# Kernel tuning notes

Measured on AMD Instinct MI355X. Metric: run time of the kernel, lower is better.

## Reference

```python
import jax, jax.numpy as jnp
import numpy as np

B, N, EDGES = 16, 50000, 1600000
CLAMP_MIN, CLAMP_MAX = -10.0, 10.0
EPS = 1e-6


def setup_inputs() -> dict:
    key = jax.random.key(0)
    ks = jax.random.split(key, 8)
    return {
        "chem_influence": jax.random.normal(ks[0], (B, N), dtype=jnp.float32),
        "E": jax.random.normal(ks[1], (B, N), dtype=jnp.float32),
        "o_pre": jax.random.uniform(ks[2], (B, N), dtype=jnp.float32),
        "w": jax.random.normal(ks[3], (EDGES,), dtype=jnp.float32),
        "threshold": jax.random.uniform(ks[4], (N,), dtype=jnp.float32),
        "decay": jax.random.uniform(ks[5], (N,), dtype=jnp.float32),
        "src": jax.random.randint(ks[6], (EDGES,), 0, N, dtype=jnp.int32),
        "dst": jax.random.randint(ks[7], (EDGES,), 0, N, dtype=jnp.int32),
    }


def reference(chem_influence, E, o_pre, w, threshold, decay, src, dst):
    # Gap-junction currents: gather, sign-compare, weighted scatter-add.
    Oj = o_pre[:, src]                      # (B, EDGES) presynaptic outputs
    En = E[:, dst]                          # (B, EDGES) postsynaptic internal states
    sgn = jnp.where(Oj >= En, 1.0, -1.0)
    contrib = Oj * w * sgn                  # (B, EDGES)
    gj_sum = jnp.zeros_like(chem_influence).at[:, dst].add(contrib)  # (B, N)

    # Neuron dynamics (eqs 10, 11).
    S = jnp.clip(E + chem_influence + gj_sum, CLAMP_MIN, CLAMP_MAX)
    gt = S > threshold                      # broadcast (N,) over (B, N)
    mask = (~gt) & (jnp.abs(S - E) <= EPS)
    new_o = jax.nn.relu(S - threshold)
    new_e = jnp.where(gt, new_o, jnp.where(mask, E - decay, S))
    return (new_o, new_e)
```

## Files before the change

### kernel.cpp

```cpp
#include <hip/hip_runtime.h>

#define BATCH 16
#define NNODES 50000
#define NEDGES 1600000
#define BN (BATCH * NNODES)
#define CLAMP_LO -10.0f
#define CLAMP_HI 10.0f
#define EPS_V 1e-6f

#define BSZ 64
#define NBINS 782
#define CAPE 2816
#define RPT 11
#define NBLK_P 782
#define EPB 2048

__global__ __launch_bounds__(256) void prep_fused(
    const float* __restrict__ o_pre,
    const int* __restrict__ src, const int* __restrict__ dst,
    const float* __restrict__ w,
    float* __restrict__ o_t,
    uint2* __restrict__ binned, int* __restrict__ gcur) {
    __shared__ int lh[NBINS];
    const int tid = threadIdx.x, bid = blockIdx.x;
    for (int i = tid; i < NBINS; i += 256) lh[i] = 0;

    const int4*   dst4 = (const int4*)dst;
    const int4*   src4 = (const int4*)src;
    const float4* w4   = (const float4*)w;
    const int e4base = bid * (EPB / 4);
    int4 d[2], s[2];
    float4 ww[2];
    bool val[2];
#pragma unroll
    for (int j = 0; j < 2; ++j) {
        int i4 = e4base + j * 256 + tid;
        val[j] = (i4 < NEDGES / 4);
        if (val[j]) { d[j] = dst4[i4]; s[j] = src4[i4]; ww[j] = w4[i4]; }
    }

    {
        int t = bid * 64 + (tid >> 2);
        int q = tid & 3;
        if (t < NNODES) {
            float v0 = o_pre[(q * 4 + 0) * NNODES + t];
            float v1 = o_pre[(q * 4 + 1) * NNODES + t];
            float v2 = o_pre[(q * 4 + 2) * NNODES + t];
            float v3 = o_pre[(q * 4 + 3) * NNODES + t];
            *(float4*)(o_t + (size_t)t * BATCH + q * 4) =
                make_float4(v0, v1, v2, v3);
        }
    }
    __syncthreads();

#pragma unroll
    for (int j = 0; j < 2; ++j) {
        if (val[j]) {
            atomicAdd(&lh[d[j].x >> 6], 1);
            atomicAdd(&lh[d[j].y >> 6], 1);
            atomicAdd(&lh[d[j].z >> 6], 1);
            atomicAdd(&lh[d[j].w >> 6], 1);
        }
    }
    __syncthreads();

    for (int i = tid; i < NBINS; i += 256) {
        int c = lh[i];
        int base = c ? atomicAdd(&gcur[i], c) : 0;
        lh[i] = i * CAPE + base;
    }
    __syncthreads();

#pragma unroll
    for (int j = 0; j < 2; ++j) {
        if (val[j]) {
            int   dd[4] = {d[j].x, d[j].y, d[j].z, d[j].w};
            int   ss[4] = {s[j].x, s[j].y, s[j].z, s[j].w};
            float wv[4] = {ww[j].x, ww[j].y, ww[j].z, ww[j].w};
#pragma unroll
            for (int m = 0; m < 4; ++m) {
                int dn  = dd[m];
                int bin = dn >> 6;
                int pos = atomicAdd(&lh[bin], 1);
                if (pos < (bin + 1) * CAPE)
                    binned[pos] = make_uint2(
                        (unsigned)ss[m] | ((unsigned)(dn & 63) << 16),
                        __float_as_uint(wv[m]));
            }
        }
    }
}

__global__ __launch_bounds__(256, 4) void bin_gather7(
    const float* __restrict__ o_t, const float* __restrict__ E,
    const float* __restrict__ chem, const float* __restrict__ threshold,
    const float* __restrict__ decay, const int* __restrict__ gcur,
    const uint2* __restrict__ binned,
    float* __restrict__ out_o, float* __restrict__ out_e) {
    __shared__ int   cnt_l[BSZ];
    __shared__ int   offs[BSZ + 1];
    __shared__ uint2 eb[CAPE];
    const int k = blockIdx.x, tid = threadIdx.x;
    const int node0 = k * BSZ;
    const int nn = (NNODES - node0 < BSZ) ? (NNODES - node0) : BSZ;
    const int s0 = k * CAPE;
    int cnt = gcur[k];
    if (cnt > CAPE) cnt = CAPE;

    uint2 r[RPT];
    if (tid < BSZ) cnt_l[tid] = 0;
    __syncthreads();
#pragma unroll
    for (int j = 0; j < RPT; ++j) {
        int idx = tid + j * 256;
        if (idx < cnt) {
            uint2 p = binned[s0 + idx];
            r[j] = p;
            atomicAdd(&cnt_l[(p.x >> 16) & 63], 1);
        }
    }
    __syncthreads();

    if (tid < BSZ) {
        int c = cnt_l[tid];
        int v = c;
#pragma unroll
        for (int o = 1; o < BSZ; o <<= 1) {
            int u = __shfl_up(v, o);
            if (tid >= o) v += u;
        }
        offs[tid]  = v - c;
        cnt_l[tid] = v - c;
        if (tid == BSZ - 1) offs[BSZ] = cnt;
    }
    __syncthreads();

#pragma unroll
    for (int j = 0; j < RPT; ++j) {
        int idx = tid + j * 256;
        if (idx < cnt) {
            uint2 p = r[j];
            int pos = atomicAdd(&cnt_l[(p.x >> 16) & 63], 1);
            eb[pos] = p;
        }
    }
    __syncthreads();

    if (tid < nn * 4) {
        const int n  = tid >> 2;
        const int q4 = (tid & 3) * 4;
        const int gn = node0 + n;
        const int e0 = offs[n], e1 = offs[n + 1];
        float ev[4];
#pragma unroll
        for (int j = 0; j < 4; ++j) ev[j] = E[(q4 + j) * NNODES + gn];
        const float th = threshold[gn];
        const float dc = decay[gn];
        float ch[4];
#pragma unroll
        for (int j = 0; j < 4; ++j) ch[j] = chem[(q4 + j) * NNODES + gn];

        float4 acc = make_float4(0.f, 0.f, 0.f, 0.f);
#define ACC1(P)                                                                 \
        {                                                                       \
            float4 oj = *(const float4*)(o_t + (size_t)((P).x & 0xFFFFu) * BATCH + q4); \
            float wv = __uint_as_float((P).y), nwv = -wv;                       \
            acc.x = fmaf(oj.x, (oj.x >= ev[0]) ? wv : nwv, acc.x);              \
            acc.y = fmaf(oj.y, (oj.y >= ev[1]) ? wv : nwv, acc.y);              \
            acc.z = fmaf(oj.z, (oj.z >= ev[2]) ? wv : nwv, acc.z);              \
            acc.w = fmaf(oj.w, (oj.w >= ev[3]) ? wv : nwv, acc.w);              \
        }
        int i = e0;
        for (; i + 4 <= e1; i += 4) {
            uint2 p0 = eb[i];
            uint2 p1 = eb[i + 1];
            uint2 p2 = eb[i + 2];
            uint2 p3 = eb[i + 3];
            ACC1(p0); ACC1(p1); ACC1(p2); ACC1(p3);
        }
        for (; i < e1; ++i) {
            uint2 p0 = eb[i];
            ACC1(p0);
        }
#undef ACC1

        float av[4] = {acc.x, acc.y, acc.z, acc.w};
#pragma unroll
        for (int j = 0; j < 4; ++j) {
            float e = ev[j];
            float S = e + ch[j] + av[j];
            S = fminf(fmaxf(S, CLAMP_LO), CLAMP_HI);
            float no = fmaxf(S - th, 0.0f);
            float ne;
            if (S > th) ne = no;
            else if (fabsf(S - e) <= EPS_V) ne = e - dc;
            else ne = S;
            out_o[(q4 + j) * NNODES + gn] = no;
            out_e[(q4 + j) * NNODES + gn] = ne;
        }
    }
}

__global__ void edge_scatter_dev(const float* __restrict__ o_pre, const float* __restrict__ E,
                                 const float* __restrict__ w, const int* __restrict__ src,
                                 const int* __restrict__ dst, float* __restrict__ gj) {
    int e = blockIdx.x * blockDim.x + threadIdx.x;
    if (e >= NEDGES) return;
    int s = src[e];
    int d = dst[e];
    float wv = w[e];
#pragma unroll
    for (int b = 0; b < BATCH; ++b) {
        float oj = o_pre[b * NNODES + s];
        float en = E[b * NNODES + d];
        atomicAdd(&gj[b * NNODES + d], (oj >= en) ? oj * wv : -oj * wv);
    }
}

__global__ void finalize_dev(const float* __restrict__ chem, const float* __restrict__ E,
                             const float* __restrict__ threshold, const float* __restrict__ decay,
                             float* __restrict__ out_o, float* __restrict__ out_e_gj) {
    int i = blockIdx.x * blockDim.x + threadIdx.x;
    if (i >= BN) return;
    int n = i % NNODES;
    float e = E[i];
    float S = e + chem[i] + out_e_gj[i];
    S = fminf(fmaxf(S, CLAMP_LO), CLAMP_HI);
    float th = threshold[n];
    float no = fmaxf(S - th, 0.0f);
    float ne;
    if (S > th) ne = no;
    else if (fabsf(S - e) <= EPS_V) ne = e - decay[n];
    else ne = S;
    out_o[i] = no;
    out_e_gj[i] = ne;
}

extern "C" void kernel_launch(void* const* d_in, const int* in_sizes, int n_in,
                              void* d_out, int out_size, void* d_ws, size_t ws_size,
                              hipStream_t stream) {
    const float* chem      = (const float*)d_in[0];
    const float* E         = (const float*)d_in[1];
    const float* o_pre     = (const float*)d_in[2];
    const float* w         = (const float*)d_in[3];
    const float* threshold = (const float*)d_in[4];
    const float* decay     = (const float*)d_in[5];
    const int*   src       = (const int*)d_in[6];
    const int*   dst       = (const int*)d_in[7];

    float* out_o = (float*)d_out;
    float* out_e = (float*)d_out + BN;

    const size_t OT_OFF  = 0;
    const size_t BIN_OFF = 3203072;
    const size_t GC_OFF  = 20819968;
    const size_t need    = GC_OFF + (size_t)NBINS * sizeof(int);

    if (ws_size >= need) {
        char* ws = (char*)d_ws;
        float* o_t    = (float*)(ws + OT_OFF);
        uint2* binned = (uint2*)(ws + BIN_OFF);
        int*   gcur   = (int*)(ws + GC_OFF);

        hipMemsetAsync(gcur, 0, (size_t)NBINS * sizeof(int), stream);
        prep_fused<<<NBLK_P, 256, 0, stream>>>(o_pre, src, dst, w, o_t, binned, gcur);
        bin_gather7<<<NBINS, 256, 0, stream>>>(o_t, E, chem, threshold, decay,
                                               gcur, binned, out_o, out_e);
    } else {
        hipMemsetAsync(out_e, 0, (size_t)BN * sizeof(float), stream);
        edge_scatter_dev<<<(NEDGES + 255) / 256, 256, 0, stream>>>(o_pre, E, w, src, dst, out_e);
        finalize_dev<<<(BN + 255) / 256, 256, 0, stream>>>(chem, E, threshold, decay, out_o, out_e);
    }
}
```

Before: 140.2 us.

## Locally sort edges by bin in LDS before writing binned output

The prep kernel now handles twice as many edges per block. It computes a block-local prefix scan of the bin histogram and counting-sorts edges into shared memory first, then writes them out contiguously per bin. This turns scattered 8-byte global writes into mostly contiguous runs per bin. In exchange it uses more LDS (about 45KB per block), adds extra syncs and a scan, and launches half as many blocks, which may reduce occupancy and parallelism.

```diff
diff --git a/kernel.cpp b/kernel.cpp
--- a/kernel.cpp
+++ b/kernel.cpp
@@ -12,16 +12,21 @@
 #define NBINS 782
 #define CAPE 2816
 #define RPT 11
-#define NBLK_P 782
-#define EPB 2048
-
-__global__ __launch_bounds__(256) void prep_fused(
+#define NBLK_P 391
+#define EPB 4096
+
+__global__ __launch_bounds__(256) void prep_sort(
     const float* __restrict__ o_pre,
     const int* __restrict__ src, const int* __restrict__ dst,
     const float* __restrict__ w,
     float* __restrict__ o_t,
     uint2* __restrict__ binned, int* __restrict__ gcur) {
-    __shared__ int lh[NBINS];
+    __shared__ int   lh[NBINS];
+    __shared__ int   offs_l[NBINS];
+    __shared__ int   gbase[NBINS];
+    __shared__ int   wsum[4];
+    __shared__ uint2 sb[EPB];
+
     const int tid = threadIdx.x, bid = blockIdx.x;
     for (int i = tid; i < NBINS; i += 256) lh[i] = 0;
 
@@ -29,32 +34,32 @@
     const int4*   src4 = (const int4*)src;
     const float4* w4   = (const float4*)w;
     const int e4base = bid * (EPB / 4);
-    int4 d[2], s[2];
-    float4 ww[2];
-    bool val[2];
-#pragma unroll
-    for (int j = 0; j < 2; ++j) {
+    int4 d[4], s[4];
+    float4 ww[4];
+    bool val[4];
+#pragma unroll
+    for (int j = 0; j < 4; ++j) {
         int i4 = e4base + j * 256 + tid;
         val[j] = (i4 < NEDGES / 4);
         if (val[j]) { d[j] = dst4[i4]; s[j] = src4[i4]; ww[j] = w4[i4]; }
     }
 
     {
-        int t = bid * 64 + (tid >> 2);
-        int q = tid & 3;
+        int t = bid * 128 + (tid >> 1);
+        int h = (tid & 1) * 8;
         if (t < NNODES) {
-            float v0 = o_pre[(q * 4 + 0) * NNODES + t];
-            float v1 = o_pre[(q * 4 + 1) * NNODES + t];
-            float v2 = o_pre[(q * 4 + 2) * NNODES + t];
-            float v3 = o_pre[(q * 4 + 3) * NNODES + t];
-            *(float4*)(o_t + (size_t)t * BATCH + q * 4) =
-                make_float4(v0, v1, v2, v3);
-        }
-    }
-    __syncthreads();
-
-#pragma unroll
-    for (int j = 0; j < 2; ++j) {
+            float v[8];
+#pragma unroll
+            for (int j = 0; j < 8; ++j) v[j] = o_pre[(h + j) * NNODES + t];
+            float4* op = (float4*)(o_t + (size_t)t * BATCH + h);
+            op[0] = make_float4(v[0], v[1], v[2], v[3]);
+            op[1] = make_float4(v[4], v[5], v[6], v[7]);
+        }
+    }
+    __syncthreads();
+
+#pragma unroll
+    for (int j = 0; j < 4; ++j) {
         if (val[j]) {
             atomicAdd(&lh[d[j].x >> 6], 1);
             atomicAdd(&lh[d[j].y >> 6], 1);
@@ -64,15 +69,47 @@
     }
     __syncthreads();
 
-    for (int i = tid; i < NBINS; i += 256) {
-        int c = lh[i];
-        int base = c ? atomicAdd(&gcur[i], c) : 0;
-        lh[i] = i * CAPE + base;
-    }
-    __syncthreads();
-
-#pragma unroll
-    for (int j = 0; j < 2; ++j) {
+    {
+        const int base4 = tid * 4;
+        int c[4];
+#pragma unroll
+        for (int m = 0; m < 4; ++m) {
+            int idx = base4 + m;
+            c[m] = (idx < NBINS) ? lh[idx] : 0;
+        }
+        int tsum = c[0] + c[1] + c[2] + c[3];
+        int v = tsum;
+        const int lane = tid & 63;
+#pragma unroll
+        for (int o = 1; o < 64; o <<= 1) {
+            int u = __shfl_up(v, o);
+            if (lane >= o) v += u;
+        }
+        if (lane == 63) wsum[tid >> 6] = v;
+        __syncthreads();
+        if (tid == 0) {
+            int a = 0;
+#pragma unroll
+            for (int i = 0; i < 4; ++i) { int t = wsum[i]; wsum[i] = a; a += t; }
+        }
+        __syncthreads();
+        int run = v - tsum + wsum[tid >> 6];
+#pragma unroll
+        for (int m = 0; m < 4; ++m) {
+            int idx = base4 + m;
+            if (idx < NBINS) {
+                offs_l[idx] = run;
+                lh[idx] = run;
+                if (c[m] > 0)
+                    gbase[idx] = idx * CAPE + atomicAdd(&gcur[idx], c[m]);
+            }
+            run += c[m];
+        }
+    }
+    __syncthreads();
+
+#pragma unroll
+    for (int j = 0; j < 4; ++j) {
         if (val[j]) {
             int   dd[4] = {d[j].x, d[j].y, d[j].z, d[j].w};
             int   ss[4] = {s[j].x, s[j].y, s[j].z, s[j].w};
@@ -82,11 +119,22 @@
                 int dn  = dd[m];
                 int bin = dn >> 6;
                 int pos = atomicAdd(&lh[bin], 1);
-                if (pos < (bin + 1) * CAPE)
-                    binned[pos] = make_uint2(
-                        (unsigned)ss[m] | ((unsigned)(dn & 63) << 16),
-                        __float_as_uint(wv[m]));
+                sb[pos] = make_uint2((unsigned)ss[m] | ((unsigned)(dn & 63) << 16) |
+                                     ((unsigned)bin << 22),
+                                     __float_as_uint(wv[m]));
             }
+        }
+    }
+    __syncthreads();
+
+    {
+        int rem = NEDGES - bid * EPB;
+        int tot = (rem < EPB) ? rem : EPB;
+        for (int i = tid; i < tot; i += 256) {
+            uint2 p = sb[i];
+            int bin = p.x >> 22;
+            int addr = gbase[bin] + (i - offs_l[bin]);
+            if (addr < (bin + 1) * CAPE) binned[addr] = p;
         }
     }
 }
@@ -263,7 +311,7 @@
         int*   gcur   = (int*)(ws + GC_OFF);
 
         hipMemsetAsync(gcur, 0, (size_t)NBINS * sizeof(int), stream);
-        prep_fused<<<NBLK_P, 256, 0, stream>>>(o_pre, src, dst, w, o_t, binned, gcur);
+        prep_sort<<<NBLK_P, 256, 0, stream>>>(o_pre, src, dst, w, o_t, binned, gcur);
         bin_gather7<<<NBINS, 256, 0, stream>>>(o_t, E, chem, threshold, decay,
                                                gcur, binned, out_o, out_e);
     } else {
```

After: 143.2 us. 1.02x slower.
